# Kernel optimization log

Measured on AMD Instinct MI355X. Metric: run time of the kernel, lower is better.

## Reference

```python
import jax, jax.numpy as jnp
import numpy as np

B, C, H = 16, 256, 128   # batch, channels (in==out, depthwise), spatial
K, S, P = 3, 2, 1        # kernel, stride, padding (the shape-consistent _Transition config)
LEAVES = 4               # levels=2 -> levels**2


def dwconv(x, w, b, stride, pad):
    # depthwise conv: w is [C,1,K,K] (torch OIHW with groups=C)
    out = jax.lax.conv_general_dilated(
        x, w, (stride, stride), [(pad, pad), (pad, pad)],
        dimension_numbers=('NCHW', 'OIHW', 'NCHW'),
        feature_group_count=x.shape[1])
    return out + b[None, :, None, None]


def maxpool(x, k, s, p):
    # matches nn.MaxPool2d (padding acts as -inf for max)
    return jax.lax.reduce_window(
        x, -jnp.inf, jax.lax.max,
        (1, 1, k, k), (1, 1, s, s),
        [(0, 0), (0, 0), (p, p), (p, p)])


def setup_inputs() -> dict:
    key = jax.random.key(0)
    k0, k1, k2, k3 = jax.random.split(key, 4)
    std = (2.0 / (K * K * C)) ** 0.5  # matches the module's normal_(0, sqrt(2/n)) init
    x = jax.random.normal(k0, (B, C, H, H), jnp.float32)
    maxgate = jax.random.normal(k1, (C, 1, K, K), jnp.float32) * std
    pconvs = jax.random.normal(k2, (C, 1, K, K, LEAVES), jnp.float32) * std  # dw=True
    pgates = jax.random.normal(k3, (C, 1, K, K, 3), jnp.float32) * std       # b=False: (leaves+levels)//2 = 3
    mb = jnp.zeros((C,), jnp.float32)
    pbs = jnp.zeros((C, LEAVES), jnp.float32)
    gbs = jnp.zeros((C, 3), jnp.float32)
    return dict(x=x, maxgate=maxgate, mb=mb, pconvs=pconvs, pbs=pbs,
                pgates=pgates, gbs=gbs)


def reference(x, maxgate, mb, pconvs, pbs, pgates, gbs):
    # max branch: maxpool * depthwise gate conv
    out = maxpool(x, K, S, P) * dwconv(x, maxgate, mb, S, P)

    # leaf stage: 2 sigmoid-gated pool pairs (b=False -> gate2 = 1 - gate1)
    # NOTE: code indexes pgates.select(4, c*2) with gbs.select(1, c)
    leaves = []
    for c in range(LEAVES // 2):
        g1 = jax.nn.sigmoid(dwconv(x, pgates[..., 2 * c], gbs[:, c], S, P))
        p1 = dwconv(x, pconvs[..., 2 * c], pbs[:, 2 * c], S, P)
        p2 = dwconv(x, pconvs[..., 2 * c + 1], pbs[:, 2 * c + 1], S, P)
        leaves.append(g1 * p1)
        leaves.append((1.0 - g1) * p2)

    n0 = leaves[0] + leaves[1]
    n1 = leaves[2] + leaves[3]

    # node stage (kernel_size==3 -> no F.pad); b=False reuses pgates[..., leaves//2 + n] = pgates[...,2]
    g = jax.nn.sigmoid(dwconv(n0, pgates[..., LEAVES // 2], gbs[:, 2], 1, P))
    out = out + n0 * g + n1 * (1.0 - g)
    return out
```

## Files before the change

### kernel.cpp

```cpp
#include <hip/hip_runtime.h>
#include <math.h>

#define TB   512
#define HH   128
#define OHW  64
#define TR   32
#define NT   2
#define XR   69
#define XC   136
#define N0R  34
#define N0C  68

__device__ __forceinline__ float sigmoidf(float z) {
    return 1.0f / (1.0f + __expf(-z));
}

__global__ __launch_bounds__(TB) void fused_densenet_kernel(
    const float* __restrict__ x,
    const float* __restrict__ maxgate,
    const float* __restrict__ mb,
    const float* __restrict__ pconvs,
    const float* __restrict__ pbs,
    const float* __restrict__ pgates,
    const float* __restrict__ gbs,
    float* __restrict__ out)
{
    __shared__ float xs[XR][XC];
    __shared__ float n0s[N0R][N0C];

    const int t     = threadIdx.x;
    const int bid   = blockIdx.x;
    const int tile  = bid & (NT - 1);
    const int plane = bid >> 1;
    const int c     = plane & 255;
    const int r0    = tile * TR;

    float ws[7][9];
#pragma unroll
    for (int i = 0; i < 9; ++i) {
        ws[0][i] = maxgate[c * 9  + i];
        ws[1][i] = pconvs [c * 36 + i * 4 + 0];
        ws[2][i] = pconvs [c * 36 + i * 4 + 1];
        ws[3][i] = pconvs [c * 36 + i * 4 + 2];
        ws[4][i] = pconvs [c * 36 + i * 4 + 3];
        ws[5][i] = pgates [c * 27 + i * 3 + 0];
        ws[6][i] = pgates [c * 27 + i * 3 + 2];
    }
    const float bmax = mb[c];
    const float bp0 = pbs[c * 4 + 0], bp1 = pbs[c * 4 + 1];
    const float bp2 = pbs[c * 4 + 2], bp3 = pbs[c * 4 + 3];
    const float bg0 = gbs[c * 3 + 0];
    const float bg1 = gbs[c * 3 + 1];
    const float bg2 = gbs[c * 3 + 2];

    const float* xplane = x + (size_t)plane * (HH * HH);
    const int ir0 = 2 * r0 - 3;
    for (int s = t; s < XR * 34; s += TB) {
        const int rr = s / 34;
        const int qq = s - rr * 34;
        float4 v = make_float4(0.f, 0.f, 0.f, 0.f);
        const int ir = ir0 + rr;
        if (qq >= 1 && qq <= 32 && (unsigned)ir < (unsigned)HH) {
            v = *reinterpret_cast<const float4*>(xplane + ir * HH + (qq - 1) * 4);
        }
        *reinterpret_cast<float4*>(&xs[rr][qq * 4]) = v;
    }
    __syncthreads();

    if (t < 196) {
        int lrr, lc;
        if (t < 66)        { lrr = 0;        lc = t;       }
        else if (t < 132)  { lrr = N0R - 1;  lc = t - 66;  }
        else { const int i = t - 132; lrr = 1 + (i >> 1); lc = (i & 1) ? 65 : 0; }
        const int gr = r0 - 1 + lrr;
        const int gc = lc - 1;
        float n0v = 0.f;
        if ((unsigned)gr < (unsigned)OHW && (unsigned)gc < (unsigned)OHW) {
            float ag = 0.f, a0 = 0.f, a1 = 0.f;
#pragma unroll
            for (int dr = 0; dr < 3; ++dr)
#pragma unroll
                for (int dc = 0; dc < 3; ++dc) {
                    const float v = xs[2 * lrr + dr][2 * lc + dc + 1];
                    const int i = dr * 3 + dc;
                    ag += v * ws[5][i];
                    a0 += v * ws[1][i];
                    a1 += v * ws[2][i];
                }
            const float sg = sigmoidf(ag + bg0);
            n0v = sg * (a0 + bp0) + (1.f - sg) * (a1 + bp1);
        }
        n0s[lrr][lc] = n0v;
    }

    const int lc64 = t & 63;
    const int wq   = t >> 6;
    float out1[4], n1[4], n0k[4];
#pragma unroll
    for (int k = 0; k < 4; ++k) {
        const int lr = wq + 8 * k;
        const int gr = r0 + lr;
        const int gc = lc64;

        float w9[9];
#pragma unroll
        for (int dr = 0; dr < 3; ++dr)
#pragma unroll
            for (int dc = 0; dc < 3; ++dc)
                w9[dr * 3 + dc] = xs[2 * lr + dr + 2][2 * lc64 + dc + 3];

        float mp = -INFINITY;
        float amax = 0.f, a0 = 0.f, a1 = 0.f, a2 = 0.f, a3 = 0.f;
        float ag0 = 0.f, ag2 = 0.f;
#pragma unroll
        for (int i = 0; i < 9; ++i) {
            const int dr = i / 3, dc = i % 3;
            const float v = w9[i];
            amax += v * ws[0][i];
            a0   += v * ws[1][i];
            a1   += v * ws[2][i];
            a2   += v * ws[3][i];
            a3   += v * ws[4][i];
            ag0  += v * ws[5][i];
            ag2  += v * ws[6][i];
            const bool valid = ((gr > 0) | (dr > 0)) & ((gc > 0) | (dc > 0));
            mp = fmaxf(mp, valid ? v : -INFINITY);
        }
        const float sg0 = sigmoidf(ag0 + bg0);
        const float n0v = sg0 * (a0 + bp0) + (1.f - sg0) * (a1 + bp1);
        n0k[k] = n0v;
        n0s[lr + 1][lc64 + 1] = n0v;
        const float sg1 = sigmoidf(ag2 + bg1);
        n1[k]   = sg1 * (a2 + bp2) + (1.f - sg1) * (a3 + bp3);
        out1[k] = mp * (amax + bmax);
    }
    __syncthreads();

    float* oplane = out + (size_t)plane * (OHW * OHW);
#pragma unroll
    for (int k = 0; k < 4; ++k) {
        const int lr = wq + 8 * k;
        float ag = 0.f;
#pragma unroll
        for (int dr = 0; dr < 3; ++dr)
            ag += n0s[lr + dr][lc64]     * ws[6][3 * dr]
                + n0s[lr + dr][lc64 + 1] * ws[6][3 * dr + 1]
                + n0s[lr + dr][lc64 + 2] * ws[6][3 * dr + 2];
        const float g = sigmoidf(ag + bg2);
        const float r = out1[k] + n0k[k] * g + n1[k] * (1.f - g);
        __builtin_nontemporal_store(r, &oplane[(r0 + lr) * OHW + lc64]);
    }
}

extern "C" void kernel_launch(void* const* d_in, const int* in_sizes, int n_in,
                              void* d_out, int out_size, void* d_ws, size_t ws_size,
                              hipStream_t stream) {
    const float* x       = (const float*)d_in[0];
    const float* maxgate = (const float*)d_in[1];
    const float* mb      = (const float*)d_in[2];
    const float* pconvs  = (const float*)d_in[3];
    const float* pbs     = (const float*)d_in[4];
    const float* pgates  = (const float*)d_in[5];
    const float* gbs     = (const float*)d_in[6];
    float* out           = (float*)d_out;

    const int blocks = 16 * 256 * NT;
    fused_densenet_kernel<<<blocks, TB, 0, stream>>>(
        x, maxgate, mb, pconvs, pbs, pgates, gbs, out);
}
```

Baseline: 86.89 us.

## Compute two adjacent output columns per thread with vectorized shared-memory loads

Each thread now produces two horizontally adjacent outputs instead of one, loading a float plus a float4 per input row so that the overlapping column is shared between both 3x3 windows. The n0 halo is shifted by one column so interior n0 writes, node-stage reads and output stores can use 2-wide vector accesses. Launch bounds are tightened to request higher occupancy. This trades more live registers per thread (14 accumulators) for fewer LDS instructions and less redundant loading, and with 512 threads the occupancy hint may force register spills.

New measurement: 87.02 us. About the same (+0.1%).

```diff
diff --git a/kernel.cpp b/kernel.cpp
--- a/kernel.cpp
+++ b/kernel.cpp
@@ -11,11 +11,13 @@
 #define N0R  34
 #define N0C  68
 
+typedef float f32x2 __attribute__((ext_vector_type(2)));
+
 __device__ __forceinline__ float sigmoidf(float z) {
     return 1.0f / (1.0f + __expf(-z));
 }
 
-__global__ __launch_bounds__(TB) void fused_densenet_kernel(
+__global__ __launch_bounds__(TB, 8) void fused_densenet_kernel(
     const float* __restrict__ x,
     const float* __restrict__ maxgate,
     const float* __restrict__ mb,
@@ -68,12 +70,12 @@
     __syncthreads();
 
     if (t < 196) {
-        int lrr, lc;
-        if (t < 66)        { lrr = 0;        lc = t;       }
-        else if (t < 132)  { lrr = N0R - 1;  lc = t - 66;  }
-        else { const int i = t - 132; lrr = 1 + (i >> 1); lc = (i & 1) ? 65 : 0; }
+        int lrr, li;
+        if (t < 66)        { lrr = 0;        li = t + 1;       }
+        else if (t < 132)  { lrr = N0R - 1;  li = t - 66 + 1;  }
+        else { const int i = t - 132; lrr = 1 + (i >> 1); li = (i & 1) ? 66 : 1; }
         const int gr = r0 - 1 + lrr;
-        const int gc = lc - 1;
+        const int gc = li - 2;
         float n0v = 0.f;
         if ((unsigned)gr < (unsigned)OHW && (unsigned)gc < (unsigned)OHW) {
             float ag = 0.f, a0 = 0.f, a1 = 0.f;
@@ -81,7 +83,7 @@
             for (int dr = 0; dr < 3; ++dr)
 #pragma unroll
                 for (int dc = 0; dc < 3; ++dc) {
-                    const float v = xs[2 * lrr + dr][2 * lc + dc + 1];
+                    const float v = xs[2 * lrr + dr][2 * gc + dc + 3];
                     const int i = dr * 3 + dc;
                     ag += v * ws[5][i];
                     a0 += v * ws[1][i];
@@ -90,65 +92,78 @@
             const float sg = sigmoidf(ag + bg0);
             n0v = sg * (a0 + bp0) + (1.f - sg) * (a1 + bp1);
         }
-        n0s[lrr][lc] = n0v;
+        n0s[lrr][li] = n0v;
     }
 
-    const int lc64 = t & 63;
-    const int wq   = t >> 6;
-    float out1[4], n1[4], n0k[4];
+    const int p  = t & 31;
+    const int g0 = t >> 5;
+    float out1[2][2], n1v[2][2];
+
 #pragma unroll
-    for (int k = 0; k < 4; ++k) {
-        const int lr = wq + 8 * k;
+    for (int k = 0; k < 2; ++k) {
+        const int lr = g0 + 16 * k;
         const int gr = r0 + lr;
-        const int gc = lc64;
 
-        float w9[9];
+        float a[7][2];
 #pragma unroll
-        for (int dr = 0; dr < 3; ++dr)
+        for (int ci = 0; ci < 7; ++ci) { a[ci][0] = 0.f; a[ci][1] = 0.f; }
+        float mp0 = -INFINITY, mp1 = -INFINITY;
+
 #pragma unroll
-            for (int dc = 0; dc < 3; ++dc)
-                w9[dr * 3 + dc] = xs[2 * lr + dr + 2][2 * lc64 + dc + 3];
+        for (int dr = 0; dr < 3; ++dr) {
+            const int xr = 2 * lr + 2 + dr;
+            const float  v0 = xs[xr][4 * p + 3];
+            const float4 vv = *reinterpret_cast<const float4*>(&xs[xr][4 * p + 4]);
 
-        float mp = -INFINITY;
-        float amax = 0.f, a0 = 0.f, a1 = 0.f, a2 = 0.f, a3 = 0.f;
-        float ag0 = 0.f, ag2 = 0.f;
+            const bool rowok = (gr > 0) | (dr > 0);
+            const float h0 = fmaxf(fmaxf((p > 0) ? v0 : -INFINITY, vv.x), vv.y);
+            const float h1 = fmaxf(fmaxf(vv.y, vv.z), vv.w);
+            mp0 = fmaxf(mp0, rowok ? h0 : -INFINITY);
+            mp1 = fmaxf(mp1, rowok ? h1 : -INFINITY);
+
 #pragma unroll
-        for (int i = 0; i < 9; ++i) {
-            const int dr = i / 3, dc = i % 3;
-            const float v = w9[i];
-            amax += v * ws[0][i];
-            a0   += v * ws[1][i];
-            a1   += v * ws[2][i];
-            a2   += v * ws[3][i];
-            a3   += v * ws[4][i];
-            ag0  += v * ws[5][i];
-            ag2  += v * ws[6][i];
-            const bool valid = ((gr > 0) | (dr > 0)) & ((gc > 0) | (dc > 0));
-            mp = fmaxf(mp, valid ? v : -INFINITY);
+            for (int ci = 0; ci < 7; ++ci) {
+                a[ci][0] += v0   * ws[ci][3 * dr] + vv.x * ws[ci][3 * dr + 1] + vv.y * ws[ci][3 * dr + 2];
+                a[ci][1] += vv.y * ws[ci][3 * dr] + vv.z * ws[ci][3 * dr + 1] + vv.w * ws[ci][3 * dr + 2];
+            }
         }
-        const float sg0 = sigmoidf(ag0 + bg0);
-        const float n0v = sg0 * (a0 + bp0) + (1.f - sg0) * (a1 + bp1);
-        n0k[k] = n0v;
-        n0s[lr + 1][lc64 + 1] = n0v;
-        const float sg1 = sigmoidf(ag2 + bg1);
-        n1[k]   = sg1 * (a2 + bp2) + (1.f - sg1) * (a3 + bp3);
-        out1[k] = mp * (amax + bmax);
+
+        const float sg0a = sigmoidf(a[5][0] + bg0);
+        const float sg0b = sigmoidf(a[5][1] + bg0);
+        const float n0a = sg0a * (a[1][0] + bp0) + (1.f - sg0a) * (a[2][0] + bp1);
+        const float n0b = sg0b * (a[1][1] + bp0) + (1.f - sg0b) * (a[2][1] + bp1);
+        *reinterpret_cast<f32x2*>(&n0s[lr + 1][2 * p + 2]) = (f32x2){ n0a, n0b };
+
+        const float sg1a = sigmoidf(a[6][0] + bg1);
+        const float sg1b = sigmoidf(a[6][1] + bg1);
+        n1v[k][0] = sg1a * (a[3][0] + bp2) + (1.f - sg1a) * (a[4][0] + bp3);
+        n1v[k][1] = sg1b * (a[3][1] + bp2) + (1.f - sg1b) * (a[4][1] + bp3);
+        out1[k][0] = mp0 * (a[0][0] + bmax);
+        out1[k][1] = mp1 * (a[0][1] + bmax);
     }
     __syncthreads();
 
     float* oplane = out + (size_t)plane * (OHW * OHW);
 #pragma unroll
-    for (int k = 0; k < 4; ++k) {
-        const int lr = wq + 8 * k;
-        float ag = 0.f;
+    for (int k = 0; k < 2; ++k) {
+        const int lr = g0 + 16 * k;
+        float ag0 = 0.f, ag1 = 0.f;
+        float n0c0 = 0.f, n0c1 = 0.f;
 #pragma unroll
-        for (int dr = 0; dr < 3; ++dr)
-            ag += n0s[lr + dr][lc64]     * ws[6][3 * dr]
-                + n0s[lr + dr][lc64 + 1] * ws[6][3 * dr + 1]
-                + n0s[lr + dr][lc64 + 2] * ws[6][3 * dr + 2];
-        const float g = sigmoidf(ag + bg2);
-        const float r = out1[k] + n0k[k] * g + n1[k] * (1.f - g);
-        __builtin_nontemporal_store(r, &oplane[(r0 + lr) * OHW + lc64]);
+        for (int dr = 0; dr < 3; ++dr) {
+            const float  e0  = n0s[lr + dr][2 * p + 1];
+            const f32x2  mid = *reinterpret_cast<const f32x2*>(&n0s[lr + dr][2 * p + 2]);
+            const float  e3  = n0s[lr + dr][2 * p + 4];
+            ag0 += e0     * ws[6][3 * dr] + mid.x * ws[6][3 * dr + 1] + mid.y * ws[6][3 * dr + 2];
+            ag1 += mid.x  * ws[6][3 * dr] + mid.y * ws[6][3 * dr + 1] + e3    * ws[6][3 * dr + 2];
+            if (dr == 1) { n0c0 = mid.x; n0c1 = mid.y; }
+        }
+        const float ga = sigmoidf(ag0 + bg2);
+        const float gb = sigmoidf(ag1 + bg2);
+        const float r0v = out1[k][0] + n0c0 * ga + n1v[k][0] * (1.f - ga);
+        const float r1v = out1[k][1] + n0c1 * gb + n1v[k][1] * (1.f - gb);
+        __builtin_nontemporal_store((f32x2){ r0v, r1v },
+            reinterpret_cast<f32x2*>(&oplane[(r0 + lr) * OHW + 2 * p]));
     }
 }
 
```
